# Performance work log

Measured on AMD Instinct MI355X. Metric: run time of the kernel, lower is better.

## Reference

```python
import jax, jax.numpy as jnp
import numpy as np

HIDDEN = 1024
NUM_HEADS = 16
HEAD_DIM = HIDDEN // NUM_HEADS


def setup_inputs() -> dict:
    key = jax.random.key(0)
    ks = jax.random.split(key, 10)
    B, T, S = 2, 2048, 2048
    sc = 1.0 / np.sqrt(HIDDEN)
    inp = {
        "tgt": jax.random.normal(ks[0], (B, T, HIDDEN), jnp.float32),
        "src": jax.random.normal(ks[1], (B, S, HIDDEN), jnp.float32),
        # per-head projection weights stacked: [H, in_dim, head_dim]
        "Wq": jax.random.normal(ks[2], (NUM_HEADS, HIDDEN, HEAD_DIM), jnp.float32) * sc,
        "bq": jnp.zeros((NUM_HEADS, HEAD_DIM), jnp.float32),
        "Wk": jax.random.normal(ks[3], (NUM_HEADS, HIDDEN, HEAD_DIM), jnp.float32) * sc,
        "bk": jnp.zeros((NUM_HEADS, HEAD_DIM), jnp.float32),
        "Wv": jax.random.normal(ks[4], (NUM_HEADS, HIDDEN, HEAD_DIM), jnp.float32) * sc,
        "bv": jnp.zeros((NUM_HEADS, HEAD_DIM), jnp.float32),
        "Wo": jax.random.normal(ks[5], (HIDDEN, HIDDEN), jnp.float32) * sc,
        "bo": jnp.zeros((HIDDEN,), jnp.float32),
    }
    return inp


def reference(tgt, src, Wq, bq, Wk, bk, Wv, bv, Wo, bo):
    # Per-head linear projections (vectorized over heads)
    q = jnp.einsum("btd,hdk->bhtk", tgt, Wq) + bq[None, :, None, :]  # [B,H,T,Dh]
    k = jnp.einsum("bsd,hdk->bhsk", src, Wk) + bk[None, :, None, :]  # [B,H,S,Dh]
    v = jnp.einsum("bsd,hdk->bhsk", src, Wv) + bv[None, :, None, :]  # [B,H,S,Dh]
    scale = 1.0 / jnp.sqrt(jnp.asarray(HEAD_DIM, q.dtype))
    scores = jnp.einsum("bhtk,bhsk->bhts", q, k) * scale  # [B,H,T,S]
    weights = jax.nn.softmax(scores, axis=-1)
    out = jnp.einsum("bhts,bhsk->bhtk", weights, v)  # [B,H,T,Dh]
    # concat heads along last dim (head order matches torch cat)
    B, H, T, Dh = out.shape
    h = out.transpose(0, 2, 1, 3).reshape(B, T, H * Dh)
    return h @ Wo + bo
```

## Files before the change

kernel.cpp:

```cpp
#include <hip/hip_runtime.h>

typedef _Float16 f16;
typedef __attribute__((ext_vector_type(4))) _Float16 f16x4;
typedef __attribute__((ext_vector_type(8))) _Float16 f16x8;
typedef __attribute__((ext_vector_type(4))) float f32x4;

constexpr int HID = 1024, NH = 16, DH = 64, BB = 2, TT = 2048, SS = 2048;
constexpr float SCL = 0.18033688011112042f;

__device__ __forceinline__ void gl_lds16(const void* g, void* l) {
  __builtin_amdgcn_global_load_lds(
      (const __attribute__((address_space(1))) void*)g,
      (__attribute__((address_space(3))) void*)l, 16, 0, 0);
}

#define VMCNT(N) asm volatile("s_waitcnt vmcnt(" #N ")" ::: "memory")

#if __has_builtin(__builtin_amdgcn_exp2f)
#define EXP2(x) __builtin_amdgcn_exp2f(x)
#else
#define EXP2(x) exp2f(x)
#endif

__global__ __launch_bounds__(256) void k_cvt_act(const float* __restrict__ in,
                                                 f16* __restrict__ out, int n) {
  int i = (blockIdx.x * 256 + threadIdx.x) * 4;
  if (i < n) {
    float4 v = *(const float4*)(in + i);
    f16x4 o; o[0] = (f16)v.x; o[1] = (f16)v.y; o[2] = (f16)v.z; o[3] = (f16)v.w;
    *(f16x4*)(out + i) = o;
  }
}

__global__ __launch_bounds__(256) void k_cvt_w(const float* __restrict__ in,
                                               f16* __restrict__ out, int C,
                                               float scale) {
  __shared__ f16 t[64 * 72];
  int c0 = blockIdx.x * 64, d0 = blockIdx.y * 64, slab = blockIdx.z;
  const float* ip = in + (size_t)slab * 1024 * C;
  int tid = threadIdx.x;
  int r = tid >> 4, cq = (tid & 15) * 4;
  for (int rr = 0; rr < 64; rr += 16) {
    float4 v = *(const float4*)(ip + (size_t)(d0 + r + rr) * C + (c0 + cq));
    t[(cq + 0) * 72 + r + rr] = (f16)(v.x * scale);
    t[(cq + 1) * 72 + r + rr] = (f16)(v.y * scale);
    t[(cq + 2) * 72 + r + rr] = (f16)(v.z * scale);
    t[(cq + 3) * 72 + r + rr] = (f16)(v.w * scale);
  }
  __syncthreads();
  int c = tid >> 2, dq = (tid & 3) * 16;
  f16* op = out + (size_t)(slab * C + c0 + c) * 1024 + d0 + dq;
  *(f16x8*)op = *(const f16x8*)&t[c * 72 + dq];
  *(f16x8*)(op + 8) = *(const f16x8*)&t[c * 72 + dq + 8];
}

__global__ __launch_bounds__(256) void k_gemm_qkv(
    const f16* __restrict__ tgt16, const f16* __restrict__ src16,
    const f16* __restrict__ wq, const f16* __restrict__ wk,
    const f16* __restrict__ wv, const float* __restrict__ bq,
    const float* __restrict__ bk, const float* __restrict__ bv,
    f16* __restrict__ Qo, f16* __restrict__ Ko, f16* __restrict__ Vo) {
  __shared__ f16 lA[128 * 64];
  __shared__ f16 lB[128 * 64];
  const int tid = threadIdx.x;
  const int lane = tid & 63, hi = lane >> 4, t16 = lane & 15;
  const int w = tid >> 6;
  const int wr = (w >> 1) * 64, wc = (w & 1) * 64;
  const int i = blockIdx.x;
  const int xcd = i & 7, j = i >> 3;
  const int z = j % 3;
  const int r = j / 3;
  const int m0 = (xcd * 4 + (r & 3)) * 128, n0 = (r >> 2) * 128;
  const f16* A = z ? src16 : tgt16;
  const f16* Bt = (z == 0) ? wq : ((z == 1) ? wk : wv);
  const float* bias = (z == 0) ? bq : ((z == 1) ? bk : bv);
  const float bscale = (z == 0) ? SCL : 1.0f;

  f32x4 acc[4][4];
#pragma unroll
  for (int a = 0; a < 4; a++)
#pragma unroll
    for (int bq_ = 0; bq_ < 4; bq_++) acc[a][bq_] = (f32x4){0.f, 0.f, 0.f, 0.f};

  for (int kt = 0; kt < 16; ++kt) {
#pragma unroll
    for (int it = 0; it < 4; ++it) {
      int u = it * 256 + tid, row = u >> 3, un = u & 7;
      int gc = kt * 64 + ((un ^ (row & 7)) << 3);
      gl_lds16(A + (size_t)(m0 + row) * 1024 + gc, (char*)lA + u * 16);
      gl_lds16(Bt + (size_t)(n0 + row) * 1024 + gc, (char*)lB + u * 16);
    }
    __syncthreads();
#pragma unroll
    for (int ks = 0; ks < 2; ++ks) {
      f16x8 af[4], bf[4];
#pragma unroll
      for (int mi = 0; mi < 4; mi++) {
        int rr = wr + mi * 16 + t16;
        af[mi] = *(const f16x8*)&lA[rr * 64 + (((ks * 4 + hi) ^ (rr & 7)) << 3)];
      }
#pragma unroll
      for (int ni = 0; ni < 4; ni++) {
        int rr = wc + ni * 16 + t16;
        bf[ni] = *(const f16x8*)&lB[rr * 64 + (((ks * 4 + hi) ^ (rr & 7)) << 3)];
      }
      __builtin_amdgcn_s_setprio(1);
#pragma unroll
      for (int mi = 0; mi < 4; mi++)
#pragma unroll
        for (int ni = 0; ni < 4; ni++)
          acc[mi][ni] = __builtin_amdgcn_mfma_f32_16x16x32_f16(
              af[mi], bf[ni], acc[mi][ni], 0, 0, 0);
      __builtin_amdgcn_s_setprio(0);
    }
    __syncthreads();
  }

  if (z < 2) {
    f16* outp = z ? Ko : Qo;
#pragma unroll
    for (int mi = 0; mi < 4; mi++)
#pragma unroll
      for (int ni = 0; ni < 4; ni++)
#pragma unroll
        for (int rg = 0; rg < 4; rg++) {
          int m = m0 + wr + mi * 16 + hi * 4 + rg;
          int n = n0 + wc + ni * 16 + t16;
          outp[(size_t)m * 1024 + n] = (f16)(acc[mi][ni][rg] + bias[n] * bscale);
        }
  } else {
#pragma unroll
    for (int mi = 0; mi < 4; mi++)
#pragma unroll
      for (int ni = 0; ni < 4; ni++)
#pragma unroll
        for (int rg = 0; rg < 4; rg++) {
          int m = m0 + wr + mi * 16 + hi * 4 + rg;
          int n = n0 + wc + ni * 16 + t16;
          int b = m >> 11, s = m & 2047;
          Vo[(((size_t)(b * NH + (n >> 6)) * DH + (n & 63)) << 11) + s] =
              (f16)(acc[mi][ni][rg] + bias[n]);
        }
  }
}

__global__ __launch_bounds__(256) void k_gemm_o(const f16* __restrict__ A,
                                                const f16* __restrict__ Bt,
                                                const float* __restrict__ bias,
                                                float* __restrict__ outp) {
  __shared__ f16 lA[128 * 64];
  __shared__ f16 lB[64 * 64];
  const int tid = threadIdx.x;
  const int lane = tid & 63, hi = lane >> 4, t16 = lane & 15;
  const int w = tid >> 6;
  const int wr = (w >> 1) * 64, wc = (w & 1) * 32;
  const int i = blockIdx.x;
  const int xcd = i & 7, j = i >> 3;
  const int m0 = (xcd * 4 + (j & 3)) * 128, n0 = (j >> 2) * 64;

  f32x4 acc[4][2];
#pragma unroll
  for (int a = 0; a < 4; a++)
#pragma unroll
    for (int bq_ = 0; bq_ < 2; bq_++) acc[a][bq_] = (f32x4){0.f, 0.f, 0.f, 0.f};

  for (int kt = 0; kt < 16; ++kt) {
#pragma unroll
    for (int it = 0; it < 4; ++it) {
      int u = it * 256 + tid, row = u >> 3, un = u & 7;
      int gc = kt * 64 + ((un ^ (row & 7)) << 3);
      gl_lds16(A + (size_t)(m0 + row) * 1024 + gc, (char*)lA + u * 16);
    }
#pragma unroll
    for (int it = 0; it < 2; ++it) {
      int u = it * 256 + tid, row = u >> 3, un = u & 7;
      int gc = kt * 64 + ((un ^ (row & 7)) << 3);
      gl_lds16(Bt + (size_t)(n0 + row) * 1024 + gc, (char*)lB + u * 16);
    }
    __syncthreads();
#pragma unroll
    for (int ks = 0; ks < 2; ++ks) {
      f16x8 af[4], bf[2];
#pragma unroll
      for (int mi = 0; mi < 4; mi++) {
        int rr = wr + mi * 16 + t16;
        af[mi] = *(const f16x8*)&lA[rr * 64 + (((ks * 4 + hi) ^ (rr & 7)) << 3)];
      }
#pragma unroll
      for (int ni = 0; ni < 2; ni++) {
        int rr = wc + ni * 16 + t16;
        bf[ni] = *(const f16x8*)&lB[rr * 64 + (((ks * 4 + hi) ^ (rr & 7)) << 3)];
      }
      __builtin_amdgcn_s_setprio(1);
#pragma unroll
      for (int mi = 0; mi < 4; mi++)
#pragma unroll
        for (int ni = 0; ni < 2; ni++)
          acc[mi][ni] = __builtin_amdgcn_mfma_f32_16x16x32_f16(
              af[mi], bf[ni], acc[mi][ni], 0, 0, 0);
      __builtin_amdgcn_s_setprio(0);
    }
    __syncthreads();
  }

#pragma unroll
  for (int mi = 0; mi < 4; mi++)
#pragma unroll
    for (int ni = 0; ni < 2; ni++)
#pragma unroll
      for (int rg = 0; rg < 4; rg++) {
        int m = m0 + wr + mi * 16 + hi * 4 + rg;
        int n = n0 + wc + ni * 16 + t16;
        outp[(size_t)m * 1024 + n] = acc[mi][ni][rg] + bias[n];
      }
}

__global__ __launch_bounds__(256) void k_attn(const f16* __restrict__ Q,
                                              const f16* __restrict__ K,
                                              const f16* __restrict__ Vt,
                                              f16* __restrict__ Hout) {
  __shared__ f16 lK[3][64 * 64];
  __shared__ f16 lV[3][64 * 64];
  const int tid = threadIdx.x;
  const int lane = tid & 63, hi = lane >> 4, t16 = lane & 15;
  const int w = tid >> 6;
  const int id = blockIdx.y * 16 + blockIdx.x;
  const int bh = (id & 7) * 4 + ((id >> 3) & 3);
  const int b = bh >> 4, h = bh & 15;
  const int tq = (id >> 5) * 128 + w * 32;

  f16x8 qa[2][2];
#pragma unroll
  for (int g = 0; g < 2; ++g)
#pragma unroll
    for (int ks = 0; ks < 2; ++ks)
      qa[g][ks] = *(const f16x8*)(Q + (size_t)(b * TT + tq + g * 16 + t16) * HID +
                                  h * DH + ks * 32 + hi * 8);
#pragma unroll
  for (int g = 0; g < 2; ++g)
#pragma unroll
    for (int ks = 0; ks < 2; ++ks) asm volatile("" : "+v"(qa[g][ks]));

  float lrow[2] = {0.f, 0.f};
  f32x4 o[2][4];
#pragma unroll
  for (int g = 0; g < 2; ++g)
#pragma unroll
    for (int dc = 0; dc < 4; ++dc) o[g][dc] = (f32x4){0.f, 0.f, 0.f, 0.f};

  auto STAGE = [&](int s, int sb) {
#pragma unroll
    for (int it = 0; it < 2; ++it) {
      int u = it * 256 + tid, row = u >> 3, un = u & 7;
      int kc = (un ^ (row & 7)) << 3;
      gl_lds16(K + (size_t)(b * SS + sb * 64 + row) * HID + h * DH + kc,
               (char*)&lK[s][0] + u * 16);
      gl_lds16(Vt + ((size_t)(b * NH + h) * DH + row) * SS + sb * 64 + kc,
               (char*)&lV[s][0] + u * 16);
    }
  };

  STAGE(0, 0);
  STAGE(1, 1);
  int cs = 0;
  for (int i = 0; i < 32; ++i) {
    if (i < 31) { VMCNT(4); } else { VMCNT(0); }
    __builtin_amdgcn_s_barrier();
    __builtin_amdgcn_sched_barrier(0);
    int ns = cs + 2; if (ns >= 3) ns -= 3;
    if (i + 2 < 32) STAGE(ns, i + 2);

    f16x8 kb[4][2];
#pragma unroll
    for (int sb = 0; sb < 4; ++sb) {
      int r = sb * 16 + t16;
#pragma unroll
      for (int ks = 0; ks < 2; ++ks)
        kb[sb][ks] = *(const f16x8*)&lK[cs][r * 64 + (((ks * 4 + hi) ^ (r & 7)) << 3)];
    }
    f32x4 sc[4][2];
#pragma unroll
    for (int sb = 0; sb < 4; ++sb)
#pragma unroll
      for (int g = 0; g < 2; ++g) sc[sb][g] = (f32x4){0.f, 0.f, 0.f, 0.f};
    __builtin_amdgcn_s_setprio(1);
#pragma unroll
    for (int sb = 0; sb < 4; ++sb)
#pragma unroll
      for (int g = 0; g < 2; ++g)
#pragma unroll
        for (int ks = 0; ks < 2; ++ks)
          sc[sb][g] = __builtin_amdgcn_mfma_f32_16x16x32_f16(
              kb[sb][ks], qa[g][ks], sc[sb][g], 0, 0, 0);
    __builtin_amdgcn_s_setprio(0);

    f16x4 pf[2][4];
#pragma unroll
    for (int g = 0; g < 2; ++g) {
#pragma unroll
      for (int sb = 0; sb < 4; ++sb) {
        float p0 = EXP2(sc[sb][g][0]);
        float p1 = EXP2(sc[sb][g][1]);
        float p2 = EXP2(sc[sb][g][2]);
        float p3 = EXP2(sc[sb][g][3]);
        lrow[g] += (p0 + p1) + (p2 + p3);
        f16x4 pv; pv[0] = (f16)p0; pv[1] = (f16)p1; pv[2] = (f16)p2; pv[3] = (f16)p3;
        pf[g][sb] = pv;
      }
    }

    f16x4 vf[4][4];
#pragma unroll
    for (int dc = 0; dc < 4; ++dc) {
#pragma unroll
      for (int sk = 0; sk < 4; ++sk) {
        int chunk = ((2 * sk + (hi >> 1)) ^ (t16 & 7));
        vf[dc][sk] = *(const f16x4*)&lV[cs][(dc * 16 + t16) * 64 + chunk * 8 + (hi & 1) * 4];
      }
    }

    __builtin_amdgcn_s_setprio(1);
#pragma unroll
    for (int g = 0; g < 2; ++g)
#pragma unroll
      for (int dc = 0; dc < 4; ++dc)
#pragma unroll
        for (int sk = 0; sk < 4; ++sk)
          o[g][dc] = __builtin_amdgcn_mfma_f32_16x16x16f16(vf[dc][sk], pf[g][sk],
                                                           o[g][dc], 0, 0, 0);
    __builtin_amdgcn_s_setprio(0);

    cs = (cs == 2) ? 0 : cs + 1;
  }

#pragma unroll
  for (int g = 0; g < 2; ++g) {
    float l = lrow[g];
    l += __shfl_xor(l, 16);
    l += __shfl_xor(l, 32);
    float rinv = 1.0f / l;
#pragma unroll
    for (int dc = 0; dc < 4; ++dc) {
      f16x4 ov;
#pragma unroll
      for (int rg = 0; rg < 4; ++rg) ov[rg] = (f16)(o[g][dc][rg] * rinv);
      *(f16x4*)(Hout + (size_t)(b * TT + tq + g * 16 + t16) * HID + h * DH +
                dc * 16 + hi * 4) = ov;
    }
  }
}

extern "C" void kernel_launch(void* const* d_in, const int* in_sizes, int n_in,
                              void* d_out, int out_size, void* d_ws, size_t ws_size,
                              hipStream_t stream) {
  const float* tgt = (const float*)d_in[0];
  const float* src = (const float*)d_in[1];
  const float* Wq = (const float*)d_in[2];
  const float* bq = (const float*)d_in[3];
  const float* Wk = (const float*)d_in[4];
  const float* bk = (const float*)d_in[5];
  const float* Wv = (const float*)d_in[6];
  const float* bv = (const float*)d_in[7];
  const float* Wo = (const float*)d_in[8];
  const float* bo = (const float*)d_in[9];
  float* out = (float*)d_out;

  char* ws = (char*)d_ws;
  f16* tgt16 = (f16*)(ws);
  f16* src16 = (f16*)(ws + (8u << 20));
  f16* wq16 = (f16*)(ws + (16u << 20));
  f16* wk16 = (f16*)(ws + (18u << 20));
  f16* wv16 = (f16*)(ws + (20u << 20));
  f16* wo16 = (f16*)(ws + (22u << 20));
  f16* Q16 = (f16*)(ws + (24u << 20));
  f16* K16 = (f16*)(ws + (32u << 20));
  f16* Vt16 = (f16*)(ws + (40u << 20));
  f16* h16 = (f16*)(ws + (48u << 20));

  k_cvt_act<<<4096, 256, 0, stream>>>(tgt, tgt16, BB * TT * HID);
  k_cvt_act<<<4096, 256, 0, stream>>>(src, src16, BB * SS * HID);
  k_cvt_w<<<dim3(1, 16, 16), 256, 0, stream>>>(Wq, wq16, 64, SCL);
  k_cvt_w<<<dim3(1, 16, 16), 256, 0, stream>>>(Wk, wk16, 64, 1.0f);
  k_cvt_w<<<dim3(1, 16, 16), 256, 0, stream>>>(Wv, wv16, 64, 1.0f);
  k_cvt_w<<<dim3(16, 16, 1), 256, 0, stream>>>(Wo, wo16, 1024, 1.0f);

  k_gemm_qkv<<<768, 256, 0, stream>>>(tgt16, src16, wq16, wk16, wv16,
                                      bq, bk, bv, Q16, K16, Vt16);

  k_attn<<<dim3(16, 32), 256, 0, stream>>>(Q16, K16, Vt16, h16);

  k_gemm_o<<<512, 256, 0, stream>>>(h16, wo16, bo, out);
}
```

Measured before the change: 221.9 us.

## Double-buffer GEMM LDS tiles and merge conversion kernels into fewer launches

Both projection GEMMs now use two LDS buffers, prefetching the next K-tile through global_load_lds while MFMAs run on the current one, with an explicit vmcnt wait and barrier per step. The six conversion launches are merged into one activation-conversion kernel with 8-wide stores and one weight-transpose kernel that dispatches on block index. The QKV block-to-tile mapping changes from a modulo-3 interleave to contiguous groups of 32 per projection, which alters L2 and XCD locality. Doubling LDS per block may lower occupancy, and waiting on vmcnt(0) at the end of each step limits how much load latency the prefetch can hide.

```diff
diff --git a/kernel.cpp b/kernel.cpp
--- a/kernel.cpp
+++ b/kernel.cpp
@@ -22,21 +22,42 @@
 #define EXP2(x) exp2f(x)
 #endif
 
-__global__ __launch_bounds__(256) void k_cvt_act(const float* __restrict__ in,
-                                                 f16* __restrict__ out, int n) {
-  int i = (blockIdx.x * 256 + threadIdx.x) * 4;
-  if (i < n) {
-    float4 v = *(const float4*)(in + i);
-    f16x4 o; o[0] = (f16)v.x; o[1] = (f16)v.y; o[2] = (f16)v.z; o[3] = (f16)v.w;
-    *(f16x4*)(out + i) = o;
-  }
-}
-
-__global__ __launch_bounds__(256) void k_cvt_w(const float* __restrict__ in,
-                                               f16* __restrict__ out, int C,
-                                               float scale) {
+__global__ __launch_bounds__(256) void k_cvt_act_all(
+    const float* __restrict__ tgt, const float* __restrict__ src,
+    f16* __restrict__ tgt16, f16* __restrict__ src16) {
+  const int n_each = BB * TT * HID;
+  int i = (blockIdx.x * 256 + threadIdx.x) * 8;
+  const float* in = tgt;
+  f16* out = tgt16;
+  if (i >= n_each) { in = src; out = src16; i -= n_each; }
+  float4 a = *(const float4*)(in + i);
+  float4 b = *(const float4*)(in + i + 4);
+  f16x8 o;
+  o[0] = (f16)a.x; o[1] = (f16)a.y; o[2] = (f16)a.z; o[3] = (f16)a.w;
+  o[4] = (f16)b.x; o[5] = (f16)b.y; o[6] = (f16)b.z; o[7] = (f16)b.w;
+  *(f16x8*)(out + i) = o;
+}
+
+__global__ __launch_bounds__(256) void k_cvt_w_all(
+    const float* __restrict__ Wq, const float* __restrict__ Wk,
+    const float* __restrict__ Wv, const float* __restrict__ Wo,
+    f16* __restrict__ wq16, f16* __restrict__ wk16, f16* __restrict__ wv16,
+    f16* __restrict__ wo16) {
   __shared__ f16 t[64 * 72];
-  int c0 = blockIdx.x * 64, d0 = blockIdx.y * 64, slab = blockIdx.z;
+  const int x = blockIdx.x, wsel = x >> 8, idx = x & 255;
+  const float* in;
+  f16* out;
+  int C, c0, d0, slab;
+  float scale = 1.0f;
+  if (wsel < 3) {
+    in = (wsel == 0) ? Wq : ((wsel == 1) ? Wk : Wv);
+    out = (wsel == 0) ? wq16 : ((wsel == 1) ? wk16 : wv16);
+    if (wsel == 0) scale = SCL;
+    C = 64; c0 = 0; d0 = (idx & 15) * 64; slab = idx >> 4;
+  } else {
+    in = Wo; out = wo16;
+    C = 1024; c0 = (idx & 15) * 64; d0 = (idx >> 4) * 64; slab = 0;
+  }
   const float* ip = in + (size_t)slab * 1024 * C;
   int tid = threadIdx.x;
   int r = tid >> 4, cq = (tid & 15) * 4;
@@ -60,16 +81,15 @@
     const f16* __restrict__ wv, const float* __restrict__ bq,
     const float* __restrict__ bk, const float* __restrict__ bv,
     f16* __restrict__ Qo, f16* __restrict__ Ko, f16* __restrict__ Vo) {
-  __shared__ f16 lA[128 * 64];
-  __shared__ f16 lB[128 * 64];
+  __shared__ f16 lA[2][128 * 64];
+  __shared__ f16 lB[2][128 * 64];
   const int tid = threadIdx.x;
   const int lane = tid & 63, hi = lane >> 4, t16 = lane & 15;
   const int w = tid >> 6;
   const int wr = (w >> 1) * 64, wc = (w & 1) * 64;
   const int i = blockIdx.x;
   const int xcd = i & 7, j = i >> 3;
-  const int z = j % 3;
-  const int r = j / 3;
+  const int z = j >> 5, r = j & 31;
   const int m0 = (xcd * 4 + (r & 3)) * 128, n0 = (r >> 2) * 128;
   const f16* A = z ? src16 : tgt16;
   const f16* Bt = (z == 0) ? wq : ((z == 1) ? wk : wv);
@@ -80,29 +100,36 @@
 #pragma unroll
   for (int a = 0; a < 4; a++)
 #pragma unroll
-    for (int bq_ = 0; bq_ < 4; bq_++) acc[a][bq_] = (f32x4){0.f, 0.f, 0.f, 0.f};
-
-  for (int kt = 0; kt < 16; ++kt) {
+    for (int bb = 0; bb < 4; bb++) acc[a][bb] = (f32x4){0.f, 0.f, 0.f, 0.f};
+
+  auto STAGE = [&](int s, int kt) {
 #pragma unroll
     for (int it = 0; it < 4; ++it) {
       int u = it * 256 + tid, row = u >> 3, un = u & 7;
       int gc = kt * 64 + ((un ^ (row & 7)) << 3);
-      gl_lds16(A + (size_t)(m0 + row) * 1024 + gc, (char*)lA + u * 16);
-      gl_lds16(Bt + (size_t)(n0 + row) * 1024 + gc, (char*)lB + u * 16);
-    }
-    __syncthreads();
+      gl_lds16(A + (size_t)(m0 + row) * 1024 + gc, (char*)&lA[s][0] + u * 16);
+      gl_lds16(Bt + (size_t)(n0 + row) * 1024 + gc, (char*)&lB[s][0] + u * 16);
+    }
+  };
+
+  STAGE(0, 0);
+  VMCNT(0);
+  __builtin_amdgcn_s_barrier();
+  int cur = 0;
+  for (int kt = 0; kt < 16; ++kt) {
+    if (kt < 15) STAGE(cur ^ 1, kt + 1);
 #pragma unroll
     for (int ks = 0; ks < 2; ++ks) {
       f16x8 af[4], bf[4];
 #pragma unroll
       for (int mi = 0; mi < 4; mi++) {
         int rr = wr + mi * 16 + t16;
-        af[mi] = *(const f16x8*)&lA[rr * 64 + (((ks * 4 + hi) ^ (rr & 7)) << 3)];
+        af[mi] = *(const f16x8*)&lA[cur][rr * 64 + (((ks * 4 + hi) ^ (rr & 7)) << 3)];
       }
 #pragma unroll
       for (int ni = 0; ni < 4; ni++) {
         int rr = wc + ni * 16 + t16;
-        bf[ni] = *(const f16x8*)&lB[rr * 64 + (((ks * 4 + hi) ^ (rr & 7)) << 3)];
+        bf[ni] = *(const f16x8*)&lB[cur][rr * 64 + (((ks * 4 + hi) ^ (rr & 7)) << 3)];
       }
       __builtin_amdgcn_s_setprio(1);
 #pragma unroll
@@ -113,7 +140,9 @@
               af[mi], bf[ni], acc[mi][ni], 0, 0, 0);
       __builtin_amdgcn_s_setprio(0);
     }
-    __syncthreads();
+    VMCNT(0);
+    __builtin_amdgcn_s_barrier();
+    cur ^= 1;
   }
 
   if (z < 2) {
@@ -148,8 +177,8 @@
                                                 const f16* __restrict__ Bt,
                                                 const float* __restrict__ bias,
                                                 float* __restrict__ outp) {
-  __shared__ f16 lA[128 * 64];
-  __shared__ f16 lB[64 * 64];
+  __shared__ f16 lA[2][128 * 64];
+  __shared__ f16 lB[2][64 * 64];
   const int tid = threadIdx.x;
   const int lane = tid & 63, hi = lane >> 4, t16 = lane & 15;
   const int w = tid >> 6;
@@ -162,34 +191,41 @@
 #pragma unroll
   for (int a = 0; a < 4; a++)
 #pragma unroll
-    for (int bq_ = 0; bq_ < 2; bq_++) acc[a][bq_] = (f32x4){0.f, 0.f, 0.f, 0.f};
-
-  for (int kt = 0; kt < 16; ++kt) {
+    for (int bb = 0; bb < 2; bb++) acc[a][bb] = (f32x4){0.f, 0.f, 0.f, 0.f};
+
+  auto STAGE = [&](int s, int kt) {
 #pragma unroll
     for (int it = 0; it < 4; ++it) {
       int u = it * 256 + tid, row = u >> 3, un = u & 7;
       int gc = kt * 64 + ((un ^ (row & 7)) << 3);
-      gl_lds16(A + (size_t)(m0 + row) * 1024 + gc, (char*)lA + u * 16);
+      gl_lds16(A + (size_t)(m0 + row) * 1024 + gc, (char*)&lA[s][0] + u * 16);
     }
 #pragma unroll
     for (int it = 0; it < 2; ++it) {
       int u = it * 256 + tid, row = u >> 3, un = u & 7;
       int gc = kt * 64 + ((un ^ (row & 7)) << 3);
-      gl_lds16(Bt + (size_t)(n0 + row) * 1024 + gc, (char*)lB + u * 16);
-    }
-    __syncthreads();
+      gl_lds16(Bt + (size_t)(n0 + row) * 1024 + gc, (char*)&lB[s][0] + u * 16);
+    }
+  };
+
+  STAGE(0, 0);
+  VMCNT(0);
+  __builtin_amdgcn_s_barrier();
+  int cur = 0;
+  for (int kt = 0; kt < 16; ++kt) {
+    if (kt < 15) STAGE(cur ^ 1, kt + 1);
 #pragma unroll
     for (int ks = 0; ks < 2; ++ks) {
       f16x8 af[4], bf[2];
 #pragma unroll
       for (int mi = 0; mi < 4; mi++) {
         int rr = wr + mi * 16 + t16;
-        af[mi] = *(const f16x8*)&lA[rr * 64 + (((ks * 4 + hi) ^ (rr & 7)) << 3)];
+        af[mi] = *(const f16x8*)&lA[cur][rr * 64 + (((ks * 4 + hi) ^ (rr & 7)) << 3)];
       }
 #pragma unroll
       for (int ni = 0; ni < 2; ni++) {
         int rr = wc + ni * 16 + t16;
-        bf[ni] = *(const f16x8*)&lB[rr * 64 + (((ks * 4 + hi) ^ (rr & 7)) << 3)];
+        bf[ni] = *(const f16x8*)&lB[cur][rr * 64 + (((ks * 4 + hi) ^ (rr & 7)) << 3)];
       }
       __builtin_amdgcn_s_setprio(1);
 #pragma unroll
@@ -200,7 +236,9 @@
               af[mi], bf[ni], acc[mi][ni], 0, 0, 0);
       __builtin_amdgcn_s_setprio(0);
     }
-    __syncthreads();
+    VMCNT(0);
+    __builtin_amdgcn_s_barrier();
+    cur ^= 1;
   }
 
 #pragma unroll
@@ -377,12 +415,8 @@
   f16* Vt16 = (f16*)(ws + (40u << 20));
   f16* h16 = (f16*)(ws + (48u << 20));
 
-  k_cvt_act<<<4096, 256, 0, stream>>>(tgt, tgt16, BB * TT * HID);
-  k_cvt_act<<<4096, 256, 0, stream>>>(src, src16, BB * SS * HID);
-  k_cvt_w<<<dim3(1, 16, 16), 256, 0, stream>>>(Wq, wq16, 64, SCL);
-  k_cvt_w<<<dim3(1, 16, 16), 256, 0, stream>>>(Wk, wk16, 64, 1.0f);
-  k_cvt_w<<<dim3(1, 16, 16), 256, 0, stream>>>(Wv, wv16, 64, 1.0f);
-  k_cvt_w<<<dim3(16, 16, 1), 256, 0, stream>>>(Wo, wo16, 1024, 1.0f);
+  k_cvt_act_all<<<4096, 256, 0, stream>>>(tgt, src, tgt16, src16);
+  k_cvt_w_all<<<1024, 256, 0, stream>>>(Wq, Wk, Wv, Wo, wq16, wk16, wv16, wo16);
 
   k_gemm_qkv<<<768, 256, 0, stream>>>(tgt16, src16, wq16, wk16, wv16,
                                       bq, bk, bv, Q16, K16, Vt16);
```

After: 212.7 us. 1.04x faster.
